# Kernel optimization log

Measured on AMD Instinct MI355X. Metric: run time of the kernel, lower is better.

Reference implementation:

```python
import jax, jax.numpy as jnp
import numpy as np

B, S, H = 512, 100, 768
LAMB = 0.8

def setup_inputs() -> dict:
    key = jax.random.key(0)
    k1, k2, k3, k4 = jax.random.split(key, 4)
    scale = 1.0 / np.sqrt(H)
    return {
        "sent_vec": jax.random.normal(k1, (B, S, H), dtype=jnp.float32),
        "mask_cls": jnp.ones((B, S), dtype=jnp.int32),
        "W_cont": jax.random.normal(k2, (1, H), dtype=jnp.float32) * scale,
        "W_sim": jax.random.normal(k3, (H, H), dtype=jnp.float32) * scale,
        "W_rel": jax.random.normal(k4, (H, H), dtype=jnp.float32) * scale,
        "b_matrix": jnp.zeros((1, 1), dtype=jnp.float32),
    }

def reference(sent_vec, mask_cls, W_cont, W_sim, W_rel, b_matrix):
    # sent_vec: [B,S,H], mask_cls: [B,S] (all ones -> true_dim == S)
    m = mask_cls.astype(sent_vec.dtype)                       # [B,S]
    mask2 = m[:, :, None] * m[:, None, :]                     # mask_my_own [B,S,S]

    # Score_Cont[b,i,j] = W_cont . sent_vec[b,i]
    cont = jnp.einsum('h,bih->bi', W_cont[0], sent_vec)       # [B,S]
    # Score_Sim[b,i,j] = sent_i W_sim sent_j^T, masked
    sim = jnp.einsum('bih,hk,bjk->bij', sent_vec, W_sim, sent_vec) * mask2
    # Score_rel[b,i,j] = sent_i W_rel d_rep, masked
    d_rep = sent_vec.mean(axis=1)                             # [B,H]
    rel = jnp.einsum('bih,hk,bk->bi', sent_vec, W_rel, d_rep) # [B,S]

    q = jax.nn.sigmoid(rel[:, :, None] * mask2 + cont[:, :, None] + sim + b_matrix[0, 0])
    q = q * mask2                                             # [B,S,S]

    # D = diag(column sums of q); q @ D^{-1} divides columns by sum_vec
    sum_vec = q.sum(axis=1)                                   # [B,S]
    qD = q / sum_vec[:, None, :]                              # [B,S,S]

    I = jnp.eye(S, dtype=q.dtype)
    M = I[None, :, :] - LAMB * qD                             # [B,S,S]
    y = jnp.full((B, S, 1), 1.0 / S, dtype=q.dtype)
    # Final_score = (1-lamb) * inv(I - lamb q D^-1) @ y  (solve == inverse@mm)
    score = (1.0 - LAMB) * jnp.linalg.solve(M, y)[:, :, 0]    # [B,S]
    return score
```

## Files before the change

### kernel.cpp

```cpp
#include <hip/hip_runtime.h>
#include <math.h>

#define BB 512
#define SS 100
#define HH 768

typedef __bf16 bf16x8 __attribute__((ext_vector_type(8)));
typedef __bf16 bf16x4 __attribute__((ext_vector_type(4)));
typedef float f32x4 __attribute__((ext_vector_type(4)));

__device__ __forceinline__ void gld16(const void* g, void* l) {
    __builtin_amdgcn_global_load_lds((const __attribute__((address_space(1))) char*)g,
                                     (__attribute__((address_space(3))) char*)l, 16, 0, 0);
}

__global__ __launch_bounds__(256) void k_drep(const float* __restrict__ X,
                                              float* __restrict__ drep) {
    int b = blockIdx.x, g = blockIdx.y;
    int lane = threadIdx.x & 63, w = threadIdx.x >> 6;
    const float4* xb = (const float4*)(X + (size_t)b * SS * HH);
    int c4 = g * 64 + lane;
    float4 s = {0.f, 0.f, 0.f, 0.f};
    for (int r = w; r < SS; r += 4) {
        float4 v = xb[r * 192 + c4];
        s.x += v.x; s.y += v.y; s.z += v.z; s.w += v.w;
    }
    __shared__ float4 red[4][64];
    red[w][lane] = s;
    __syncthreads();
    if (w == 0) {
        float4 a0 = red[0][lane], a1 = red[1][lane], a2 = red[2][lane], a3 = red[3][lane];
        float4 o;
        o.x = (a0.x + a1.x + a2.x + a3.x) * (1.0f / SS);
        o.y = (a0.y + a1.y + a2.y + a3.y) * (1.0f / SS);
        o.z = (a0.z + a1.z + a2.z + a3.z) * (1.0f / SS);
        o.w = (a0.w + a1.w + a2.w + a3.w) * (1.0f / SS);
        ((float4*)(drep + (size_t)b * HH))[c4] = o;
    }
}

__global__ __launch_bounds__(256) void k_gemm_nt(const float* __restrict__ A,
                                                 const float* __restrict__ Bm,
                                                 float* __restrict__ C,
                                                 int N, int K) {
    __shared__ float As[64 * 20];
    __shared__ float Bs[64 * 20];
    int tid = threadIdx.x;
    int ty = tid >> 4, tx = tid & 15;
    int m0 = blockIdx.y * 64, n0 = blockIdx.x * 64;
    int lr = tid >> 2, lc = (tid & 3) * 4;
    float acc[4][4] = {};
    for (int kt = 0; kt < K; kt += 16) {
        *(float4*)(As + lr * 20 + lc) = *(const float4*)(A + (size_t)(m0 + lr) * K + kt + lc);
        *(float4*)(Bs + lr * 20 + lc) = *(const float4*)(Bm + (size_t)(n0 + lr) * K + kt + lc);
        __syncthreads();
        #pragma unroll
        for (int k = 0; k < 16; k += 2) {
            float2 ar[4], br[4];
            #pragma unroll
            for (int ii = 0; ii < 4; ++ii) ar[ii] = *(const float2*)(As + (ty + 16 * ii) * 20 + k);
            #pragma unroll
            for (int jj = 0; jj < 4; ++jj) br[jj] = *(const float2*)(Bs + (tx + 16 * jj) * 20 + k);
            #pragma unroll
            for (int ii = 0; ii < 4; ++ii)
                #pragma unroll
                for (int jj = 0; jj < 4; ++jj)
                    acc[ii][jj] = fmaf(ar[ii].y, br[jj].y, fmaf(ar[ii].x, br[jj].x, acc[ii][jj]));
        }
        __syncthreads();
    }
    #pragma unroll
    for (int ii = 0; ii < 4; ++ii)
        #pragma unroll
        for (int jj = 0; jj < 4; ++jj)
            C[(size_t)(m0 + ty + 16 * ii) * N + n0 + tx + 16 * jj] = acc[ii][jj];
}

__global__ __launch_bounds__(256) void k_splitw(const float* __restrict__ W,
                                                __bf16* __restrict__ th,
                                                __bf16* __restrict__ tl) {
    __shared__ float tile[32][33];
    int bn = blockIdx.x * 32, bk = blockIdx.y * 32;
    int tx = threadIdx.x & 31, ty = threadIdx.x >> 5;
    for (int r = ty; r < 32; r += 8)
        tile[r][tx] = W[(size_t)(bk + r) * HH + bn + tx];
    __syncthreads();
    for (int r = ty; r < 32; r += 8) {
        float v = tile[tx][r];
        __bf16 hv = (__bf16)v;
        size_t idx = (size_t)(bn + r) * HH + bk + tx;
        th[idx] = hv;
        tl[idx] = (__bf16)(v - (float)hv);
    }
}

__global__ __launch_bounds__(512) void k_split_contrel(const float* __restrict__ X,
                                                       const float* __restrict__ Wc,
                                                       const float* __restrict__ tmat,
                                                       const float* __restrict__ bmat,
                                                       __bf16* __restrict__ Xh,
                                                       __bf16* __restrict__ Xl,
                                                       float* __restrict__ avec,
                                                       int b_off) {
    __shared__ float4 u4[192];
    int lb = blockIdx.x, half = blockIdx.y;
    int b = b_off + lb;
    int tid = threadIdx.x, lane = tid & 63, w = tid >> 6;
    for (int c = tid; c < 192; c += 512) {
        float4 wc = ((const float4*)Wc)[c];
        float4 tm = ((const float4*)(tmat + (size_t)b * HH))[c];
        float4 o = {wc.x + tm.x, wc.y + tm.y, wc.z + tm.z, wc.w + tm.w};
        u4[c] = o;
    }
    __syncthreads();
    float b00 = bmat[0];
    const float4* xb = (const float4*)(X + (size_t)b * SS * HH);
    bf16x4* xh4 = (bf16x4*)(Xh + (size_t)lb * SS * HH);
    bf16x4* xl4 = (bf16x4*)(Xl + (size_t)lb * SS * HH);
    int rend = half * 50 + 50;
    for (int r = half * 50 + w; r < rend; r += 8) {
        float s = 0.f;
        #pragma unroll
        for (int cc = 0; cc < 3; ++cc) {
            int c = cc * 64 + lane;
            float4 v = xb[r * 192 + c];
            float4 uu = u4[c];
            s = fmaf(v.x, uu.x, fmaf(v.y, uu.y, fmaf(v.z, uu.z, fmaf(v.w, uu.w, s))));
            bf16x4 hv, lv;
            hv[0] = (__bf16)v.x; lv[0] = (__bf16)(v.x - (float)hv[0]);
            hv[1] = (__bf16)v.y; lv[1] = (__bf16)(v.y - (float)hv[1]);
            hv[2] = (__bf16)v.z; lv[2] = (__bf16)(v.z - (float)hv[2]);
            hv[3] = (__bf16)v.w; lv[3] = (__bf16)(v.w - (float)hv[3]);
            xh4[r * 192 + c] = hv;
            xl4[r * 192 + c] = lv;
        }
        #pragma unroll
        for (int off = 32; off > 0; off >>= 1) s += __shfl_down(s, off);
        if (lane == 0) avec[(size_t)b * SS + r] = s + b00;
    }
}

__global__ __launch_bounds__(256) void k_gemm1_mfma(const __bf16* __restrict__ Ah_g,
                                                    const __bf16* __restrict__ Al_g,
                                                    const __bf16* __restrict__ Bh_g,
                                                    const __bf16* __restrict__ Bl_g,
                                                    __bf16* __restrict__ Yh,
                                                    __bf16* __restrict__ Yl) {
    __shared__ __align__(16) __bf16 lds[4 * 4096];
    __bf16* As_h = lds;
    __bf16* As_l = lds + 4096;
    __bf16* Bs_h = lds + 8192;
    __bf16* Bs_l = lds + 12288;
    const int tid = threadIdx.x;
    const int wave = tid >> 6, lane = tid & 63;
    const int wy = wave >> 1, wx = wave & 1;
    const size_t m0 = (size_t)blockIdx.y * 128;
    const int n0 = blockIdx.x * 128;

    const int srow = wave * 32 + (lane >> 2);
    const int scol = (lane & 3) * 8;
    const int lds_base = wave * 1024;

    const int arow = wy * 64 + (lane & 15);
    const int brow = wx * 64 + (lane & 15);
    const int koff = (lane >> 4) * 8;

    f32x4 acc[4][4] = {};
    for (int kt = 0; kt < HH; kt += 32) {
        const size_t ga0 = (m0 + srow) * HH + kt + scol;
        const size_t ga1 = ga0 + (size_t)16 * HH;
        const size_t gb0 = (size_t)(n0 + srow) * HH + kt + scol;
        const size_t gb1 = gb0 + (size_t)16 * HH;
        gld16(Ah_g + ga0, As_h + lds_base);
        gld16(Ah_g + ga1, As_h + lds_base + 512);
        gld16(Al_g + ga0, As_l + lds_base);
        gld16(Al_g + ga1, As_l + lds_base + 512);
        gld16(Bh_g + gb0, Bs_h + lds_base);
        gld16(Bh_g + gb1, Bs_h + lds_base + 512);
        gld16(Bl_g + gb0, Bs_l + lds_base);
        gld16(Bl_g + gb1, Bs_l + lds_base + 512);
        __syncthreads();
        bf16x8 fah[4], fal[4], fbh[4], fbl[4];
        #pragma unroll
        for (int t = 0; t < 4; ++t) {
            fah[t] = *(const bf16x8*)(As_h + (arow + t * 16) * 32 + koff);
            fal[t] = *(const bf16x8*)(As_l + (arow + t * 16) * 32 + koff);
            fbh[t] = *(const bf16x8*)(Bs_h + (brow + t * 16) * 32 + koff);
            fbl[t] = *(const bf16x8*)(Bs_l + (brow + t * 16) * 32 + koff);
        }
        #pragma unroll
        for (int ti = 0; ti < 4; ++ti)
            #pragma unroll
            for (int tj = 0; tj < 4; ++tj) {
                acc[ti][tj] = __builtin_amdgcn_mfma_f32_16x16x32_bf16(fal[ti], fbh[tj], acc[ti][tj], 0, 0, 0);
                acc[ti][tj] = __builtin_amdgcn_mfma_f32_16x16x32_bf16(fah[ti], fbl[tj], acc[ti][tj], 0, 0, 0);
                acc[ti][tj] = __builtin_amdgcn_mfma_f32_16x16x32_bf16(fah[ti], fbh[tj], acc[ti][tj], 0, 0, 0);
            }
        __syncthreads();
    }
    #pragma unroll
    for (int ti = 0; ti < 4; ++ti) {
        int row0 = wy * 64 + ti * 16 + (lane >> 4) * 4;
        #pragma unroll
        for (int tj = 0; tj < 4; ++tj) {
            int col = n0 + wx * 64 + tj * 16 + (lane & 15);
            #pragma unroll
            for (int r = 0; r < 4; ++r) {
                float v = acc[ti][tj][r];
                __bf16 hv = (__bf16)v;
                size_t idx = (m0 + row0 + r) * HH + col;
                Yh[idx] = hv;
                Yl[idx] = (__bf16)(v - (float)hv);
            }
        }
    }
}

__global__ __launch_bounds__(256) void k_gemm2_mfma(const __bf16* __restrict__ Yh,
                                                    const __bf16* __restrict__ Yl,
                                                    const __bf16* __restrict__ Xh,
                                                    const __bf16* __restrict__ Xl,
                                                    const float* __restrict__ avec,
                                                    float* __restrict__ q, int b_off) {
    __shared__ __align__(16) __bf16 lds[12288];
    __bf16* As_h = lds;
    __bf16* As_l = lds + 2048;
    __bf16* Bs_h = lds + 4096;
    __bf16* Bs_l = lds + 8192;
    const int bl = blockIdx.x >> 1;
    const int rh = (blockIdx.x & 1) * 64;
    const int b = b_off + bl;
    const __bf16* Ah_g = Yh + (size_t)bl * SS * HH;
    const __bf16* Al_g = Yl + (size_t)bl * SS * HH;
    const __bf16* Bh_g = Xh + (size_t)bl * SS * HH;
    const __bf16* Bl_g = Xl + (size_t)bl * SS * HH;
    const int tid = threadIdx.x;
    const int wave = tid >> 6, lane = tid & 63;
    const int wy = wave >> 1, wx = wave & 1;

    int ar_ = rh + (tid >> 2); if (ar_ >= SS) ar_ = SS - 1;
    const int scol = (lane & 3) * 8;
    const int a_base = wave * 512;
    const int sbrow = wave * 32 + (lane >> 2);
    const int b_base = wave * 1024;
    const int br0 = sbrow < SS ? sbrow : SS - 1;
    const int br1 = (sbrow + 16) < SS ? (sbrow + 16) : SS - 1;

    const int arow = wy * 32 + (lane & 15);
    const int brow = wx * 64 + (lane & 15);
    const int koff = (lane >> 4) * 8;

    f32x4 acc[2][4] = {};
    for (int kt = 0; kt < HH; kt += 32) {
        const size_t ga  = (size_t)ar_ * HH + kt + scol;
        const size_t gb0 = (size_t)br0 * HH + kt + scol;
        const size_t gb1 = (size_t)br1 * HH + kt + scol;
        gld16(Ah_g + ga,  As_h + a_base);
        gld16(Al_g + ga,  As_l + a_base);
        gld16(Bh_g + gb0, Bs_h + b_base);
        gld16(Bh_g + gb1, Bs_h + b_base + 512);
        gld16(Bl_g + gb0, Bs_l + b_base);
        gld16(Bl_g + gb1, Bs_l + b_base + 512);
        __syncthreads();
        bf16x8 fah[2], fal[2], fbh[4], fbl[4];
        #pragma unroll
        for (int t = 0; t < 2; ++t) {
            fah[t] = *(const bf16x8*)(As_h + (arow + t * 16) * 32 + koff);
            fal[t] = *(const bf16x8*)(As_l + (arow + t * 16) * 32 + koff);
        }
        #pragma unroll
        for (int t = 0; t < 4; ++t) {
            fbh[t] = *(const bf16x8*)(Bs_h + (brow + t * 16) * 32 + koff);
            fbl[t] = *(const bf16x8*)(Bs_l + (brow + t * 16) * 32 + koff);
        }
        #pragma unroll
        for (int ti = 0; ti < 2; ++ti)
            #pragma unroll
            for (int tj = 0; tj < 4; ++tj) {
                acc[ti][tj] = __builtin_amdgcn_mfma_f32_16x16x32_bf16(fal[ti], fbh[tj], acc[ti][tj], 0, 0, 0);
                acc[ti][tj] = __builtin_amdgcn_mfma_f32_16x16x32_bf16(fah[ti], fbl[tj], acc[ti][tj], 0, 0, 0);
                acc[ti][tj] = __builtin_amdgcn_mfma_f32_16x16x32_bf16(fah[ti], fbh[tj], acc[ti][tj], 0, 0, 0);
            }
        __syncthreads();
    }
    float* qb = q + (size_t)b * SS * SS;
    const float* av = avec + (size_t)b * SS;
    #pragma unroll
    for (int ti = 0; ti < 2; ++ti) {
        int i0 = rh + wy * 32 + ti * 16 + (lane >> 4) * 4;
        if (i0 >= SS) continue;
        #pragma unroll
        for (int tj = 0; tj < 4; ++tj) {
            int j = wx * 64 + tj * 16 + (lane & 15);
            if (j >= SS) continue;
            #pragma unroll
            for (int r = 0; r < 4; ++r) {
                int i = i0 + r;
                if (i >= SS) continue;
                float v = acc[ti][tj][r] + av[i];
                qb[(size_t)i * SS + j] = 1.0f / (1.0f + __expf(-v));
            }
        }
    }
}

__global__ __launch_bounds__(128) void k_solve(const float* __restrict__ q,
                                               float* __restrict__ out) {
    __shared__ __align__(16) float m[SS * SS];
    __shared__ __align__(16) float csinv[SS];
    __shared__ __align__(16) float x0[SS], x1[SS];
    int b = blockIdx.x, tid = threadIdx.x;
    const float* qb = q + (size_t)b * SS * SS;
    for (int e4 = tid; e4 < SS * SS / 4; e4 += 128)
        *(float4*)(m + e4 * 4) = *(const float4*)(qb + (size_t)e4 * 4);
    __syncthreads();
    if (tid < SS) {
        float s = 0.f;
        for (int i = 0; i < SS; ++i) s += m[i * SS + tid];
        csinv[tid] = 0.8f / s;
        x0[tid] = 1.0f / SS;
    }
    __syncthreads();
    float4 mreg[25];
    if (tid < SS) {
        #pragma unroll
        for (int j4 = 0; j4 < 25; ++j4) {
            float4 mv = *(const float4*)(m + tid * SS + j4 * 4);
            float4 cv = *(const float4*)(csinv + j4 * 4);
            mreg[j4].x = mv.x * cv.x;
            mreg[j4].y = mv.y * cv.y;
            mreg[j4].z = mv.z * cv.z;
            mreg[j4].w = mv.w * cv.w;
        }
    } else {
        #pragma unroll
        for (int j4 = 0; j4 < 25; ++j4) mreg[j4] = float4{0, 0, 0, 0};
    }
    __syncthreads();
    #pragma unroll 1
    for (int it = 0; it < 56; ++it) {
        const float* xr = (it & 1) ? x1 : x0;
        float* xw = (it & 1) ? x0 : x1;
        if (tid < SS) {
            float sx = 0.f, sy = 0.f, sz = 0.f, sw = 0.f;
            #pragma unroll
            for (int j4 = 0; j4 < 25; ++j4) {
                float4 xv = *(const float4*)(xr + j4 * 4);
                sx = fmaf(mreg[j4].x, xv.x, sx);
                sy = fmaf(mreg[j4].y, xv.y, sy);
                sz = fmaf(mreg[j4].z, xv.z, sz);
                sw = fmaf(mreg[j4].w, xv.w, sw);
            }
            xw[tid] = 0.002f + ((sx + sy) + (sz + sw));
        }
        __syncthreads();
    }
    if (tid < SS) out[(size_t)b * SS + tid] = x0[tid];
}

extern "C" void kernel_launch(void* const* d_in, const int* in_sizes, int n_in,
                              void* d_out, int out_size, void* d_ws, size_t ws_size,
                              hipStream_t stream) {
    (void)in_sizes; (void)n_in; (void)out_size;
    const float* X    = (const float*)d_in[0];
    const float* Wc   = (const float*)d_in[2];
    const float* Wsim = (const float*)d_in[3];
    const float* Wrel = (const float*)d_in[4];
    const float* bmat = (const float*)d_in[5];
    float* out = (float*)d_out;

    char* ws = (char*)d_ws;
    size_t off = 0;
    float*  qbuf = (float*)(ws + off);  off += (size_t)BB * SS * SS * 4;
    float*  drep = (float*)(ws + off);  off += (size_t)BB * HH * 4;
    float*  tmat = (float*)(ws + off);  off += (size_t)BB * HH * 4;
    float*  avec = (float*)(ws + off);  off += (size_t)BB * SS * 4;
    __bf16* Wth  = (__bf16*)(ws + off); off += (size_t)HH * HH * 2;
    __bf16* Wtl  = (__bf16*)(ws + off); off += (size_t)HH * HH * 2;

    int CB = 512;
    while (CB > 128 && off + 4 * (size_t)CB * SS * HH * 2 > ws_size) CB >>= 1;
    size_t xsz = (size_t)CB * SS * HH * 2;
    __bf16* Xh = (__bf16*)(ws + off); off += xsz;
    __bf16* Xl = (__bf16*)(ws + off); off += xsz;
    __bf16* Yh = (__bf16*)(ws + off); off += xsz;
    __bf16* Yl = (__bf16*)(ws + off); off += xsz;

    k_drep<<<dim3(BB, 3), 256, 0, stream>>>(X, drep);
    k_gemm_nt<<<dim3(HH / 64, BB / 64), 256, 0, stream>>>(drep, Wrel, tmat, HH, HH);
    k_splitw<<<dim3(HH / 32, HH / 32), 256, 0, stream>>>(Wsim, Wth, Wtl);

    for (int c = 0; c < BB; c += CB) {
        k_split_contrel<<<dim3(CB, 2), 512, 0, stream>>>(X + (size_t)c * SS * HH, Wc, tmat, bmat, Xh, Xl, avec, c);
        k_gemm1_mfma<<<dim3(HH / 128, CB * SS / 128), 256, 0, stream>>>(Xh, Xl, Wth, Wtl, Yh, Yl);
        k_gemm2_mfma<<<2 * CB, 256, 0, stream>>>(Yh, Yl, Xh, Xl, avec, qbuf, c);
    }
    k_solve<<<BB, 128, 0, stream>>>(qbuf, out);
}
```

Baseline: 755.3 us.

## Switch both GEMMs to 32x32x16 MFMA and cover full 128x128 tile per block in gemm2

Both split-bf16 GEMM kernels move from 16x16x32 to 32x32x16 MFMA instructions, with 2x2 tiles of 32x32 per wave and two k-halves per 32-wide K step. The epilogue index mapping is rewritten to match the 32x32 accumulator layout. gemm2 now uses one block per batch element covering all 100x100 outputs, loading A and B rows once per block instead of splitting rows across two blocks. The avec values are staged in LDS. This cuts the number of LDS fragment reads per MFMA and avoids reloading the B operand twice, but it halves the gemm2 grid and wastes more padding work on the 128-wide tile.

```diff
diff --git a/kernel.cpp b/kernel.cpp
--- a/kernel.cpp
+++ b/kernel.cpp
@@ -8,6 +8,7 @@
 typedef __bf16 bf16x8 __attribute__((ext_vector_type(8)));
 typedef __bf16 bf16x4 __attribute__((ext_vector_type(4)));
 typedef float f32x4 __attribute__((ext_vector_type(4)));
+typedef float f32x16 __attribute__((ext_vector_type(16)));
 
 __device__ __forceinline__ void gld16(const void* g, void* l) {
     __builtin_amdgcn_global_load_lds((const __attribute__((address_space(1))) char*)g,
@@ -161,11 +162,11 @@
     const int scol = (lane & 3) * 8;
     const int lds_base = wave * 1024;
 
-    const int arow = wy * 64 + (lane & 15);
-    const int brow = wx * 64 + (lane & 15);
-    const int koff = (lane >> 4) * 8;
-
-    f32x4 acc[4][4] = {};
+    const int arow = wy * 64 + (lane & 31);
+    const int brow = wx * 64 + (lane & 31);
+    const int koct = (lane >> 5) * 8;
+
+    f32x16 acc[2][2] = {};
     for (int kt = 0; kt < HH; kt += 32) {
         const size_t ga0 = (m0 + srow) * HH + kt + scol;
         const size_t ga1 = ga0 + (size_t)16 * HH;
@@ -180,35 +181,41 @@
         gld16(Bl_g + gb0, Bs_l + lds_base);
         gld16(Bl_g + gb1, Bs_l + lds_base + 512);
         __syncthreads();
-        bf16x8 fah[4], fal[4], fbh[4], fbl[4];
-        #pragma unroll
-        for (int t = 0; t < 4; ++t) {
-            fah[t] = *(const bf16x8*)(As_h + (arow + t * 16) * 32 + koff);
-            fal[t] = *(const bf16x8*)(As_l + (arow + t * 16) * 32 + koff);
-            fbh[t] = *(const bf16x8*)(Bs_h + (brow + t * 16) * 32 + koff);
-            fbl[t] = *(const bf16x8*)(Bs_l + (brow + t * 16) * 32 + koff);
-        }
-        #pragma unroll
-        for (int ti = 0; ti < 4; ++ti)
-            #pragma unroll
-            for (int tj = 0; tj < 4; ++tj) {
-                acc[ti][tj] = __builtin_amdgcn_mfma_f32_16x16x32_bf16(fal[ti], fbh[tj], acc[ti][tj], 0, 0, 0);
-                acc[ti][tj] = __builtin_amdgcn_mfma_f32_16x16x32_bf16(fah[ti], fbl[tj], acc[ti][tj], 0, 0, 0);
-                acc[ti][tj] = __builtin_amdgcn_mfma_f32_16x16x32_bf16(fah[ti], fbh[tj], acc[ti][tj], 0, 0, 0);
+        #pragma unroll
+        for (int kh = 0; kh < 2; ++kh) {
+            const int ko = kh * 16 + koct;
+            bf16x8 fah[2], fal[2], fbh[2], fbl[2];
+            #pragma unroll
+            for (int t = 0; t < 2; ++t) {
+                fah[t] = *(const bf16x8*)(As_h + (arow + t * 32) * 32 + ko);
+                fal[t] = *(const bf16x8*)(As_l + (arow + t * 32) * 32 + ko);
+                fbh[t] = *(const bf16x8*)(Bs_h + (brow + t * 32) * 32 + ko);
+                fbl[t] = *(const bf16x8*)(Bs_l + (brow + t * 32) * 32 + ko);
             }
-        __syncthreads();
-    }
+            #pragma unroll
+            for (int ti = 0; ti < 2; ++ti)
+                #pragma unroll
+                for (int tj = 0; tj < 2; ++tj) {
+                    acc[ti][tj] = __builtin_amdgcn_mfma_f32_32x32x16_bf16(fal[ti], fbh[tj], acc[ti][tj], 0, 0, 0);
+                    acc[ti][tj] = __builtin_amdgcn_mfma_f32_32x32x16_bf16(fah[ti], fbl[tj], acc[ti][tj], 0, 0, 0);
+                    acc[ti][tj] = __builtin_amdgcn_mfma_f32_32x32x16_bf16(fah[ti], fbh[tj], acc[ti][tj], 0, 0, 0);
+                }
+        }
+        __syncthreads();
+    }
+    const int rbase = 4 * (lane >> 5);
+    const int colb = lane & 31;
     #pragma unroll
-    for (int ti = 0; ti < 4; ++ti) {
-        int row0 = wy * 64 + ti * 16 + (lane >> 4) * 4;
-        #pragma unroll
-        for (int tj = 0; tj < 4; ++tj) {
-            int col = n0 + wx * 64 + tj * 16 + (lane & 15);
-            #pragma unroll
-            for (int r = 0; r < 4; ++r) {
+    for (int ti = 0; ti < 2; ++ti) {
+        #pragma unroll
+        for (int tj = 0; tj < 2; ++tj) {
+            int col = n0 + wx * 64 + tj * 32 + colb;
+            #pragma unroll
+            for (int r = 0; r < 16; ++r) {
+                int row = wy * 64 + ti * 32 + (r & 3) + 8 * (r >> 2) + rbase;
                 float v = acc[ti][tj][r];
                 __bf16 hv = (__bf16)v;
-                size_t idx = (m0 + row0 + r) * HH + col;
+                size_t idx = (m0 + row) * HH + col;
                 Yh[idx] = hv;
                 Yl[idx] = (__bf16)(v - (float)hv);
             }
@@ -222,13 +229,13 @@
                                                     const __bf16* __restrict__ Xl,
                                                     const float* __restrict__ avec,
                                                     float* __restrict__ q, int b_off) {
-    __shared__ __align__(16) __bf16 lds[12288];
+    __shared__ __align__(16) __bf16 lds[4 * 4096];
+    __shared__ float av_s[SS];
     __bf16* As_h = lds;
-    __bf16* As_l = lds + 2048;
-    __bf16* Bs_h = lds + 4096;
-    __bf16* Bs_l = lds + 8192;
-    const int bl = blockIdx.x >> 1;
-    const int rh = (blockIdx.x & 1) * 64;
+    __bf16* As_l = lds + 4096;
+    __bf16* Bs_h = lds + 8192;
+    __bf16* Bs_l = lds + 12288;
+    const int bl = blockIdx.x;
     const int b = b_off + bl;
     const __bf16* Ah_g = Yh + (size_t)bl * SS * HH;
     const __bf16* Al_g = Yl + (size_t)bl * SS * HH;
@@ -237,67 +244,67 @@
     const int tid = threadIdx.x;
     const int wave = tid >> 6, lane = tid & 63;
     const int wy = wave >> 1, wx = wave & 1;
-
-    int ar_ = rh + (tid >> 2); if (ar_ >= SS) ar_ = SS - 1;
+    if (tid < SS) av_s[tid] = avec[(size_t)b * SS + tid];
+
+    const int srow_raw = wave * 32 + (lane >> 2);
     const int scol = (lane & 3) * 8;
-    const int a_base = wave * 512;
-    const int sbrow = wave * 32 + (lane >> 2);
-    const int b_base = wave * 1024;
-    const int br0 = sbrow < SS ? sbrow : SS - 1;
-    const int br1 = (sbrow + 16) < SS ? (sbrow + 16) : SS - 1;
-
-    const int arow = wy * 32 + (lane & 15);
-    const int brow = wx * 64 + (lane & 15);
-    const int koff = (lane >> 4) * 8;
-
-    f32x4 acc[2][4] = {};
+    const int lds_base = wave * 1024;
+    const int r0 = srow_raw < SS ? srow_raw : SS - 1;
+    const int r1 = (srow_raw + 16) < SS ? (srow_raw + 16) : SS - 1;
+
+    const int arow = wy * 64 + (lane & 31);
+    const int brow = wx * 64 + (lane & 31);
+    const int koct = (lane >> 5) * 8;
+
+    f32x16 acc[2][2] = {};
     for (int kt = 0; kt < HH; kt += 32) {
-        const size_t ga  = (size_t)ar_ * HH + kt + scol;
-        const size_t gb0 = (size_t)br0 * HH + kt + scol;
-        const size_t gb1 = (size_t)br1 * HH + kt + scol;
-        gld16(Ah_g + ga,  As_h + a_base);
-        gld16(Al_g + ga,  As_l + a_base);
-        gld16(Bh_g + gb0, Bs_h + b_base);
-        gld16(Bh_g + gb1, Bs_h + b_base + 512);
-        gld16(Bl_g + gb0, Bs_l + b_base);
-        gld16(Bl_g + gb1, Bs_l + b_base + 512);
-        __syncthreads();
-        bf16x8 fah[2], fal[2], fbh[4], fbl[4];
-        #pragma unroll
-        for (int t = 0; t < 2; ++t) {
-            fah[t] = *(const bf16x8*)(As_h + (arow + t * 16) * 32 + koff);
-            fal[t] = *(const bf16x8*)(As_l + (arow + t * 16) * 32 + koff);
-        }
-        #pragma unroll
-        for (int t = 0; t < 4; ++t) {
-            fbh[t] = *(const bf16x8*)(Bs_h + (brow + t * 16) * 32 + koff);
-            fbl[t] = *(const bf16x8*)(Bs_l + (brow + t * 16) * 32 + koff);
-        }
-        #pragma unroll
-        for (int ti = 0; ti < 2; ++ti)
-            #pragma unroll
-            for (int tj = 0; tj < 4; ++tj) {
-                acc[ti][tj] = __builtin_amdgcn_mfma_f32_16x16x32_bf16(fal[ti], fbh[tj], acc[ti][tj], 0, 0, 0);
-                acc[ti][tj] = __builtin_amdgcn_mfma_f32_16x16x32_bf16(fah[ti], fbl[tj], acc[ti][tj], 0, 0, 0);
-                acc[ti][tj] = __builtin_amdgcn_mfma_f32_16x16x32_bf16(fah[ti], fbh[tj], acc[ti][tj], 0, 0, 0);
+        const size_t ga0 = (size_t)r0 * HH + kt + scol;
+        const size_t ga1 = (size_t)r1 * HH + kt + scol;
+        gld16(Ah_g + ga0, As_h + lds_base);
+        gld16(Ah_g + ga1, As_h + lds_base + 512);
+        gld16(Al_g + ga0, As_l + lds_base);
+        gld16(Al_g + ga1, As_l + lds_base + 512);
+        gld16(Bh_g + ga0, Bs_h + lds_base);
+        gld16(Bh_g + ga1, Bs_h + lds_base + 512);
+        gld16(Bl_g + ga0, Bs_l + lds_base);
+        gld16(Bl_g + ga1, Bs_l + lds_base + 512);
+        __syncthreads();
+        #pragma unroll
+        for (int kh = 0; kh < 2; ++kh) {
+            const int ko = kh * 16 + koct;
+            bf16x8 fah[2], fal[2], fbh[2], fbl[2];
+            #pragma unroll
+            for (int t = 0; t < 2; ++t) {
+                fah[t] = *(const bf16x8*)(As_h + (arow + t * 32) * 32 + ko);
+                fal[t] = *(const bf16x8*)(As_l + (arow + t * 32) * 32 + ko);
+                fbh[t] = *(const bf16x8*)(Bs_h + (brow + t * 32) * 32 + ko);
+                fbl[t] = *(const bf16x8*)(Bs_l + (brow + t * 32) * 32 + ko);
             }
+            #pragma unroll
+            for (int ti = 0; ti < 2; ++ti)
+                #pragma unroll
+                for (int tj = 0; tj < 2; ++tj) {
+                    acc[ti][tj] = __builtin_amdgcn_mfma_f32_32x32x16_bf16(fal[ti], fbh[tj], acc[ti][tj], 0, 0, 0);
+                    acc[ti][tj] = __builtin_amdgcn_mfma_f32_32x32x16_bf16(fah[ti], fbl[tj], acc[ti][tj], 0, 0, 0);
+                    acc[ti][tj] = __builtin_amdgcn_mfma_f32_32x32x16_bf16(fah[ti], fbh[tj], acc[ti][tj], 0, 0, 0);
+                }
+        }
         __syncthreads();
     }
     float* qb = q + (size_t)b * SS * SS;
-    const float* av = avec + (size_t)b * SS;
+    const int rbase = 4 * (lane >> 5);
+    const int colb = lane & 31;
     #pragma unroll
     for (int ti = 0; ti < 2; ++ti) {
-        int i0 = rh + wy * 32 + ti * 16 + (lane >> 4) * 4;
-        if (i0 >= SS) continue;
-        #pragma unroll
-        for (int tj = 0; tj < 4; ++tj) {
-            int j = wx * 64 + tj * 16 + (lane & 15);
+        #pragma unroll
+        for (int tj = 0; tj < 2; ++tj) {
+            int j = wx * 64 + tj * 32 + colb;
             if (j >= SS) continue;
             #pragma unroll
-            for (int r = 0; r < 4; ++r) {
-                int i = i0 + r;
+            for (int r = 0; r < 16; ++r) {
+                int i = wy * 64 + ti * 32 + (r & 3) + 8 * (r >> 2) + rbase;
                 if (i >= SS) continue;
-                float v = acc[ti][tj][r] + av[i];
+                float v = acc[ti][tj][r] + av_s[i];
                 qb[(size_t)i * SS + j] = 1.0f / (1.0f + __expf(-v));
             }
         }
@@ -393,7 +400,7 @@
     for (int c = 0; c < BB; c += CB) {
         k_split_contrel<<<dim3(CB, 2), 512, 0, stream>>>(X + (size_t)c * SS * HH, Wc, tmat, bmat, Xh, Xl, avec, c);
         k_gemm1_mfma<<<dim3(HH / 128, CB * SS / 128), 256, 0, stream>>>(Xh, Xl, Wth, Wtl, Yh, Yl);
-        k_gemm2_mfma<<<2 * CB, 256, 0, stream>>>(Yh, Yl, Xh, Xl, avec, qbuf, c);
+        k_gemm2_mfma<<<CB, 256, 0, stream>>>(Yh, Yl, Xh, Xl, avec, qbuf, c);
     }
     k_solve<<<BB, 128, 0, stream>>>(qbuf, out);
 }
```

After: 732.4 us. 3.0% less time.
